# Kernel tuning notes

Measured on AMD Instinct MI355X. Metric: run time of the kernel, lower is better.

Reference implementation:

```python
import jax, jax.numpy as jnp
import numpy as np
from jax import lax

N_HEADS = 8
D_K = 64
D_V = 64
TEMP = float(np.sqrt(D_K))  # MixtureOfSoftMax temperature = d_k ** 0.5


def avg_pool_3x3_s2_same(x):
    """TF-style AveragePooling2D(pool=3, stride=2, padding='same'), NHWC.
    TF excludes padded elements from the average (divide by valid count)."""
    sums = lax.reduce_window(x, 0.0, lax.add, (1, 3, 3, 1), (1, 2, 2, 1), 'SAME')
    ones = jnp.ones(x.shape[:3] + (1,), x.dtype)
    cnt = lax.reduce_window(ones, 0.0, lax.add, (1, 3, 3, 1), (1, 2, 2, 1), 'SAME')
    return sums / cnt


def conv1x1(x, w, b):
    # 1x1 conv == per-pixel channel matmul
    return jnp.einsum('bhwc,cd->bhwd', x, w) + b


def setup_inputs() -> dict:
    key = jax.random.key(0)
    ks = jax.random.split(key, 6)
    C = 512
    s1 = float(np.sqrt(2.0 / (C + D_K)))  # init_weight1 std
    s3 = float(np.sqrt(2.0 / (C + D_V)))  # init_weight3 std
    return {
        'x':   jax.random.normal(ks[0], (4, 64, 64, C), jnp.float32),
        'w_q': jax.random.normal(ks[1], (C, N_HEADS * D_K), jnp.float32) * s1,
        'b_q': jnp.zeros((N_HEADS * D_K,), jnp.float32),
        'w_k': jax.random.normal(ks[2], (C, N_HEADS * D_K), jnp.float32) * s1,
        'b_k': jnp.zeros((N_HEADS * D_K,), jnp.float32),
        'w_v': jax.random.normal(ks[3], (C, N_HEADS * D_V), jnp.float32) * s3,
        'b_v': jnp.zeros((N_HEADS * D_V,), jnp.float32),
        'w_o': jax.random.normal(ks[4], (N_HEADS * D_V, C), jnp.float32) * 0.02,
        'b_o': jnp.zeros((C,), jnp.float32),
    }


def reference(x, w_q, b_q, w_k, b_k, w_v, b_v, w_o, b_o):
    BS, H, W, C = x.shape
    residual = x
    # Q from full-res x; K, V from 3x3/s2 average-pooled x (pooling=True)
    qt = conv1x1(x, w_q, b_q).reshape(BS * N_HEADS, H * W, -1)          # (B*h, N, d_k)
    xp = avg_pool_3x3_s2_same(x)                                         # (BS, H/2, W/2, C)
    kt = conv1x1(xp, w_k, b_k).reshape(BS * N_HEADS, H * W // 4, -1)     # (B*h, N/4, d_k)
    vt = conv1x1(xp, w_v, b_v).reshape(BS * N_HEADS, H * W // 4, -1)     # (B*h, N/4, d_v)
    # MixtureOfSoftMaxACF with n_mix=1: scaled dot-product softmax attention
    attn = jnp.einsum('bnd,bmd->bnm', qt, kt) / TEMP                     # (B*h, N, N/4)
    attn = jax.nn.softmax(attn, axis=-1)                                 # dropout=identity (inference)
    out = jnp.einsum('bnm,bmd->bnd', attn, vt)                           # (B*h, N, d_v)
    out = out.reshape(BS, H, W, -1)
    out = conv1x1(out, w_o, b_o)                                         # conv1x1_bn_relu (Conv2D only in call)
    return out + residual                                                # concat=False -> Add
```

## Files before the change

### kernel.cpp

```cpp
#include <hip/hip_runtime.h>
#include <hip/hip_bf16.h>
#include <math.h>

typedef short bf16x8 __attribute__((ext_vector_type(8)));
typedef float f32x4 __attribute__((ext_vector_type(4)));
typedef unsigned short u16;

__device__ inline float b2f(u16 h) {
    unsigned int u = ((unsigned int)h) << 16;
    float f;
    __builtin_memcpy(&f, &u, 4);
    return f;
}

__device__ inline u16 f2b(float f) {
    unsigned int u;
    __builtin_memcpy(&u, &f, 4);
    unsigned int lsb = (u >> 16) & 1u;
    u += 0x7fffu + lsb;
    return (u16)(u >> 16);
}

__device__ __forceinline__ void gl2lds16(const u16* g, u16* l) {
    __builtin_amdgcn_global_load_lds(
        (const __attribute__((address_space(1))) unsigned int*)g,
        (__attribute__((address_space(3))) unsigned int*)l,
        16, 0, 0);
}

#define PITCH 72

#define QSCALE 0.18033688011112042f

__global__ __launch_bounds__(256) void prep_kernel(const float* __restrict__ x,
                                                   const float* __restrict__ w0,
                                                   const float* __restrict__ w1,
                                                   const float* __restrict__ w2,
                                                   const float* __restrict__ w3,
                                                   u16* __restrict__ wt,
                                                   u16* __restrict__ xp) {
    __shared__ u16 T[64 * PITCH];
    int tid = threadIdx.x;
    if (blockIdx.x >= 256) {
        int idx = (blockIdx.x - 256) * 256 + tid;
        int c8 = idx & 63;
        int j = (idx >> 6) & 31;
        int i = (idx >> 11) & 31;
        int b = idx >> 16;
        int r0 = 2 * i, c0 = 2 * j;
        int rmax = min(r0 + 3, 64), cmax = min(c0 + 3, 64);
        float acc[8] = {};
        for (int r = r0; r < rmax; ++r)
            for (int cc = c0; cc < cmax; ++cc) {
                const float* p = &x[(size_t)((((b << 6) + r) << 6) + cc) * 512 + c8 * 8];
                float4 v0 = *(const float4*)p;
                float4 v1 = *(const float4*)(p + 4);
                acc[0] += v0.x; acc[1] += v0.y; acc[2] += v0.z; acc[3] += v0.w;
                acc[4] += v1.x; acc[5] += v1.y; acc[6] += v1.z; acc[7] += v1.w;
            }
        float inv = 1.f / (float)((rmax - r0) * (cmax - c0));
        u16 o[8];
#pragma unroll
        for (int t = 0; t < 8; ++t) o[t] = f2b(acc[t] * inv);
        *(int4*)(&xp[(size_t)idx * 8]) = *(int4*)o;
        return;
    }
    int t5 = blockIdx.x;
    int bx = t5 & 7, by = (t5 >> 3) & 7, bz = t5 >> 6;
    const float* W = bz == 0 ? w0 : bz == 1 ? w1 : bz == 2 ? w2 : w3;
    u16* WT = wt + (size_t)bz * 262144;
    int nB = bx * 64, kB = by * 64;
#pragma unroll
    for (int t = 0; t < 4; ++t) {
        int e = tid + t * 256;
        int r = e >> 4, c4 = (e & 15) * 4;
        float4 v = *(const float4*)(&W[(size_t)(kB + r) * 512 + nB + c4]);
        u16* dst = &T[r * PITCH + c4];
        dst[0] = f2b(v.x); dst[1] = f2b(v.y); dst[2] = f2b(v.z); dst[3] = f2b(v.w);
    }
    __syncthreads();
    int n = tid & 63, kg = tid >> 6;
#pragma unroll
    for (int p = 0; p < 2; ++p) {
        int k0 = (kg + p * 4) * 8;
        u16 tmp[8];
#pragma unroll
        for (int i = 0; i < 8; ++i) tmp[i] = T[(k0 + i) * PITCH + n];
        *(int4*)(&WT[(size_t)(nB + n) * 512 + kB + k0]) = *(int4*)tmp;
    }
}

template <int OM, int BN, int GY, bool AF32>
__device__ __forceinline__ void gemm_body(int bid,
                                          const void* __restrict__ Av,
                                          const u16* __restrict__ WT,
                                          const float* __restrict__ bias,
                                          const float* __restrict__ bias2res,
                                          void* __restrict__ Cv,
                                          void* __restrict__ Cv2,
                                          float oscale,
                                          u16* At, u16* Bt) {
    int tid = threadIdx.x, lane = tid & 63, wave = tid >> 6;
    int q = lane >> 4, l16 = lane & 15;
    constexpr int MI = (BN == 128) ? 2 : 1;
    int wm, wn;
    if constexpr (BN == 128) { wm = wave & 1; wn = wave >> 1; }
    else                     { wm = wave;     wn = 0; }
    int nBlk = bid / GY;
    int mBlk = bid - nBlk * GY;
    int nBase = nBlk * BN, mBase = mBlk * 64;
    f32x4 acc[MI][4] = {};

    for (int kk = 0; kk < 512; kk += 64) {
        __syncthreads();
        if constexpr (AF32) {
            const float* Af = (const float*)Av;
#pragma unroll
            for (int t = 0; t < 4; ++t) {
                int c = tid + t * 256;
                int m = c >> 4, kc = (c & 15) ^ (m & 15);
                gl2lds16((const u16*)&Af[(size_t)(mBase + m) * 512 + kk + kc * 4],
                         &At[c * 8]);
            }
        } else {
            const u16* Ab = (const u16*)Av;
#pragma unroll
            for (int t = 0; t < 2; ++t) {
                int c = tid + t * 256;
                int m = c >> 3, kc = (c & 7) ^ (m & 7);
                gl2lds16(&Ab[(size_t)(mBase + m) * 512 + kk + kc * 8], &At[c * 8]);
            }
        }
#pragma unroll
        for (int t = 0; t < BN / 32; ++t) {
            int c = tid + t * 256;
            int m = c >> 3, kc = (c & 7) ^ (m & 7);
            gl2lds16(&WT[(size_t)(nBase + m) * 512 + kk + kc * 8], &Bt[c * 8]);
        }
        __syncthreads();
#pragma unroll
        for (int ds = 0; ds < 2; ++ds) {
            bf16x8 a[MI], b[4];
#pragma unroll
            for (int i = 0; i < MI; ++i) {
                int ma = (BN == 128 ? wm * 32 : wm * 16) + i * 16 + l16;
                if constexpr (AF32) {
                    const float* Ar = (const float*)At + ma * 64;
                    int c0 = ((ds << 3) + (q << 1)) ^ (ma & 15);
                    int c1 = c0 ^ 1;
                    float4 v0 = *(const float4*)(Ar + c0 * 4);
                    float4 v1 = *(const float4*)(Ar + c1 * 4);
                    unsigned r0, r1, r2, r3;
                    asm("v_cvt_pk_bf16_f32 %0, %1, %2" : "=v"(r0) : "v"(v0.x), "v"(v0.y));
                    asm("v_cvt_pk_bf16_f32 %0, %1, %2" : "=v"(r1) : "v"(v0.z), "v"(v0.w));
                    asm("v_cvt_pk_bf16_f32 %0, %1, %2" : "=v"(r2) : "v"(v1.x), "v"(v1.y));
                    asm("v_cvt_pk_bf16_f32 %0, %1, %2" : "=v"(r3) : "v"(v1.z), "v"(v1.w));
                    int4 tmp;
                    tmp.x = (int)r0; tmp.y = (int)r1; tmp.z = (int)r2; tmp.w = (int)r3;
                    __builtin_memcpy(&a[i], &tmp, 16);
                } else {
                    a[i] = *(bf16x8*)(&At[ma * 64 + ((((ds << 2) + q) ^ (ma & 7)) << 3)]);
                }
            }
#pragma unroll
            for (int j = 0; j < 4; ++j) {
                int nb = wn * 64 + j * 16 + l16;
                b[j] = *(bf16x8*)(&Bt[nb * 64 + ((((ds << 2) + q) ^ (nb & 7)) << 3)]);
            }
#pragma unroll
            for (int i = 0; i < MI; ++i)
#pragma unroll
                for (int j = 0; j < 4; ++j)
                    acc[i][j] = __builtin_amdgcn_mfma_f32_16x16x32_bf16(a[i], b[j], acc[i][j], 0, 0, 0);
        }
    }

    bool isK = (OM != 3) || (nBase < 512);
#pragma unroll
    for (int j = 0; j < 4; ++j) {
        int col = nBase + wn * 64 + j * 16 + l16;
        float bv;
        if constexpr (OM == 3) bv = isK ? bias[col] : bias2res[col - 512];
        else bv = bias[col];
#pragma unroll
        for (int i = 0; i < MI; ++i) {
#pragma unroll
            for (int r = 0; r < 4; ++r) {
                int row = mBase + (BN == 128 ? wm * 32 : wm * 16) + i * 16 + q * 4 + r;
                float v = acc[i][j][r] + bv;
                if constexpr (OM == 1) {
                    v += bias2res[(size_t)row * 512 + col];
                    ((float*)Cv)[(size_t)row * 512 + col] = v;
                } else if constexpr (OM == 0) {
                    ((u16*)Cv)[(size_t)row * 512 + col] = f2b(v * oscale);
                } else {
                    if (isK) {
                        ((u16*)Cv)[(size_t)row * 512 + col] = f2b(v);
                    } else {
                        int colv = col - 512;
                        int g = row >> 7, m2 = ((row & 127) << 3) + (colv >> 6), d = colv & 63;
                        ((u16*)Cv2)[(size_t)((g << 6) + d) * 1024 + m2] = f2b(v);
                    }
                }
            }
        }
    }
}

__global__ __launch_bounds__(256, 4) void qkv_kernel(const float* __restrict__ x,
                                                     const u16* __restrict__ xp,
                                                     const u16* __restrict__ wT,
                                                     const float* __restrict__ b_q,
                                                     const float* __restrict__ b_k,
                                                     const float* __restrict__ b_v,
                                                     u16* __restrict__ Qw,
                                                     u16* __restrict__ Kw,
                                                     u16* __restrict__ VwT) {
    __shared__ __align__(16) u16 At[64 * 128];
    __shared__ __align__(16) u16 Bt[128 * 64];
    int gid = blockIdx.x;
    if (gid < 1024) {
        gemm_body<0, 128, 256, true>(gid, x, wT, b_q, nullptr, Qw, nullptr, QSCALE, At, Bt);
    } else {
        gemm_body<3, 64, 64, false>(gid - 1024, xp, wT + 262144, b_k, b_v, Kw, VwT, 1.0f, At, Bt);
    }
}

__global__ __launch_bounds__(256, 4) void gemm_o_kernel(const u16* __restrict__ Ow,
                                                        const u16* __restrict__ wTo,
                                                        const float* __restrict__ b_o,
                                                        const float* __restrict__ xres,
                                                        float* __restrict__ out) {
    __shared__ __align__(16) u16 At[64 * 64];
    __shared__ __align__(16) u16 Bt[128 * 64];
    gemm_body<1, 128, 256, false>(blockIdx.x, Ow, wTo, b_o, xres, out, nullptr, 1.0f, At, Bt);
}

__global__ __launch_bounds__(256, 4) void attn_kernel(const u16* __restrict__ Q,
                                                      const u16* __restrict__ K,
                                                      const u16* __restrict__ VT_g,
                                                      u16* __restrict__ O) {
    int g = blockIdx.x;
    int qtile = blockIdx.y;
    const u16* Qg = Q + (size_t)g * 262144;
    const u16* Kg = K + (size_t)g * 65536;
    const u16* Vt = VT_g + (size_t)g * 65536;
    u16* Og = O + (size_t)g * 262144;

    __shared__ __align__(16) u16 Kt[2][64 * 64];
    __shared__ __align__(16) u16 VTs[2][64 * 64];
    __shared__ __align__(16) u16 Pt[64 * 64];

    int tid = threadIdx.x, lane = tid & 63, wave = tid >> 6;
    int q = lane >> 4, l16 = lane & 15;
    int n0 = qtile * 128;
    int pkey = (l16 & 7) << 2;
    int prow = (wave * 16 + l16) * 32;
    int* Pt32 = (int*)Pt;

    bf16x8 qf[2][2];
#pragma unroll
    for (int s = 0; s < 2; ++s)
#pragma unroll
        for (int ds = 0; ds < 2; ++ds)
            qf[s][ds] = *(const bf16x8*)(
                &Qg[(size_t)(n0 + s * 64 + wave * 16 + l16) * 64 + ds * 32 + q * 8]);

    f32x4 oacc[2][4] = {};
    float rsum[2] = {0.f, 0.f};

    auto stage = [&](int buf, int kb) {
#pragma unroll
        for (int t = 0; t < 2; ++t) {
            int c = tid + t * 256;
            int m = c >> 3, kc = (c & 7) ^ (m & 7);
            gl2lds16(&Kg[(size_t)(kb * 64 + m) * 64 + kc * 8], &Kt[buf][c * 8]);
            gl2lds16(&Vt[(size_t)m * 1024 + kb * 64 + kc * 8], &VTs[buf][c * 8]);
        }
    };

    stage(0, 0);
    asm volatile("s_waitcnt vmcnt(0)" ::: "memory");
    __syncthreads();

    int cur = 0;
#pragma unroll 1
    for (int kb = 0; kb < 16; ++kb) {
        if (kb < 15) stage(cur ^ 1, kb + 1);
        const u16* KtB = Kt[cur];
        const u16* VTsB = VTs[cur];
#pragma unroll
        for (int s = 0; s < 2; ++s) {
#pragma unroll
            for (int cb = 0; cb < 4; ++cb) {
                int m = cb * 16 + l16;
                bf16x8 kf0 = *(const bf16x8*)(&KtB[m * 64 + ((q ^ (m & 7)) << 3)]);
                bf16x8 kf1 = *(const bf16x8*)(&KtB[m * 64 + (((4 + q) ^ (m & 7)) << 3)]);
                f32x4 z = {};
                __builtin_amdgcn_s_setprio(1);
                z = __builtin_amdgcn_mfma_f32_16x16x32_bf16(kf0, qf[s][0], z, 0, 0, 0);
                z = __builtin_amdgcn_mfma_f32_16x16x32_bf16(kf1, qf[s][1], z, 0, 0, 0);
                __builtin_amdgcn_s_setprio(0);
                float p0 = __builtin_amdgcn_exp2f(z[0]);
                float p1 = __builtin_amdgcn_exp2f(z[1]);
                float p2 = __builtin_amdgcn_exp2f(z[2]);
                float p3 = __builtin_amdgcn_exp2f(z[3]);
                rsum[s] += (p0 + p1) + (p2 + p3);
                unsigned w0, w1;
                asm("v_cvt_pk_bf16_f32 %0, %1, %2" : "=v"(w0) : "v"(p0), "v"(p1));
                asm("v_cvt_pk_bf16_f32 %0, %1, %2" : "=v"(w1) : "v"(p2), "v"(p3));
                int2 w;
                w.x = (int)w0;
                w.y = (int)w1;
                int pd = (cb * 8 + q * 2) ^ pkey;
                *(int2*)(&Pt32[prow + pd]) = w;
            }
#pragma unroll
            for (int ds = 0; ds < 2; ++ds) {
                int pd = (ds * 16 + q * 4) ^ pkey;
                bf16x8 ap = *(bf16x8*)(&Pt32[prow + pd]);
                __builtin_amdgcn_s_setprio(1);
#pragma unroll
                for (int db = 0; db < 4; ++db) {
                    int dd = db * 16 + l16;
                    int jj = ds * 4 + q;
                    bf16x8 vb = *(const bf16x8*)(&VTsB[dd * 64 + ((jj ^ (dd & 7)) << 3)]);
                    oacc[s][db] = __builtin_amdgcn_mfma_f32_16x16x32_bf16(ap, vb, oacc[s][db], 0, 0, 0);
                }
                __builtin_amdgcn_s_setprio(0);
            }
        }
        asm volatile("s_waitcnt vmcnt(0)" ::: "memory");
        __syncthreads();
        cur ^= 1;
    }

#pragma unroll
    for (int s = 0; s < 2; ++s) {
        float v = rsum[s];
        v += __shfl_xor(v, 16, 64);
        v += __shfl_xor(v, 32, 64);
        rsum[s] = v;
    }
    float inv[2][4];
#pragma unroll
    for (int s = 0; s < 2; ++s)
#pragma unroll
        for (int r = 0; r < 4; ++r)
            inv[s][r] = 1.f / __shfl(rsum[s], q * 4 + r, 64);
#pragma unroll
    for (int s = 0; s < 2; ++s)
#pragma unroll
        for (int db = 0; db < 4; ++db)
#pragma unroll
            for (int r = 0; r < 4; ++r) {
                int row = n0 + s * 64 + wave * 16 + q * 4 + r;
                Og[(size_t)row * 64 + db * 16 + l16] = f2b(oacc[s][db][r] * inv[s][r]);
            }
}

extern "C" void kernel_launch(void* const* d_in, const int* in_sizes, int n_in,
                              void* d_out, int out_size, void* d_ws, size_t ws_size,
                              hipStream_t stream) {
    const float* x   = (const float*)d_in[0];
    const float* w_q = (const float*)d_in[1];
    const float* b_q = (const float*)d_in[2];
    const float* w_k = (const float*)d_in[3];
    const float* b_k = (const float*)d_in[4];
    const float* w_v = (const float*)d_in[5];
    const float* b_v = (const float*)d_in[6];
    const float* w_o = (const float*)d_in[7];
    const float* b_o = (const float*)d_in[8];
    float* out = (float*)d_out;

    char* ws = (char*)d_ws;
    u16* Ow  = (u16*)(ws);
    u16* xp  = (u16*)(ws + (16ull << 20));
    u16* Qw  = (u16*)(ws + (20ull << 20));
    u16* Kw  = (u16*)(ws + (36ull << 20));
    u16* VwT = (u16*)(ws + (40ull << 20));
    u16* wT  = (u16*)(ws + (44ull << 20));

    prep_kernel<<<1280, 256, 0, stream>>>(x, w_q, w_k, w_v, w_o, wT, xp);
    qkv_kernel<<<2048, 256, 0, stream>>>(x, xp, wT, b_q, b_k, b_v, Qw, Kw, VwT);
    attn_kernel<<<dim3(32, 32), 256, 0, stream>>>(Qw, Kw, VwT, Ow);
    gemm_o_kernel<<<1024, 256, 0, stream>>>(Ow, wT + 786432, b_o, x, out);
}
```

Measured before the change: 194.5 us.

## Switch attention to 32x32x16 MFMA and keep P in registers via permlane32 swap

The attention kernel now uses 32x32x16 bf16 MFMA tiles, with each wave owning 32 query rows, in place of 16x16x32 tiles over two 64-row slices. The softmax probabilities are converted to bf16 and rearranged across lane halves with v_permlane32_swap so they can feed the P·V MFMA directly from registers. This removes the LDS round trip for P and the Pt shared buffer. The aim is to cut LDS traffic and instruction overhead, at the cost of more accumulator registers per wave and a more intricate lane mapping for rows and the row-sum reduction.

```diff
diff --git a/kernel.cpp b/kernel.cpp
--- a/kernel.cpp
+++ b/kernel.cpp
@@ -4,6 +4,7 @@
 
 typedef short bf16x8 __attribute__((ext_vector_type(8)));
 typedef float f32x4 __attribute__((ext_vector_type(4)));
+typedef float f32x16 __attribute__((ext_vector_type(16)));
 typedef unsigned short u16;
 
 __device__ inline float b2f(u16 h) {
@@ -249,25 +250,18 @@
 
     __shared__ __align__(16) u16 Kt[2][64 * 64];
     __shared__ __align__(16) u16 VTs[2][64 * 64];
-    __shared__ __align__(16) u16 Pt[64 * 64];
 
     int tid = threadIdx.x, lane = tid & 63, wave = tid >> 6;
-    int q = lane >> 4, l16 = lane & 15;
-    int n0 = qtile * 128;
-    int pkey = (l16 & 7) << 2;
-    int prow = (wave * 16 + l16) * 32;
-    int* Pt32 = (int*)Pt;
-
-    bf16x8 qf[2][2];
-#pragma unroll
-    for (int s = 0; s < 2; ++s)
-#pragma unroll
-        for (int ds = 0; ds < 2; ++ds)
-            qf[s][ds] = *(const bf16x8*)(
-                &Qg[(size_t)(n0 + s * 64 + wave * 16 + l16) * 64 + ds * 32 + q * 8]);
-
-    f32x4 oacc[2][4] = {};
-    float rsum[2] = {0.f, 0.f};
+    int l32 = lane & 31, h = lane >> 5;
+    int w0 = qtile * 128 + wave * 32;
+
+    bf16x8 qf[4];
+#pragma unroll
+    for (int j = 0; j < 4; ++j)
+        qf[j] = *(const bf16x8*)(&Qg[(size_t)(w0 + l32) * 64 + j * 16 + h * 8]);
+
+    f32x16 oacc[2] = {};
+    float rsum = 0.f;
 
     auto stage = [&](int buf, int kb) {
 #pragma unroll
@@ -290,73 +284,65 @@
         const u16* KtB = Kt[cur];
         const u16* VTsB = VTs[cur];
 #pragma unroll
-        for (int s = 0; s < 2; ++s) {
-#pragma unroll
-            for (int cb = 0; cb < 4; ++cb) {
-                int m = cb * 16 + l16;
-                bf16x8 kf0 = *(const bf16x8*)(&KtB[m * 64 + ((q ^ (m & 7)) << 3)]);
-                bf16x8 kf1 = *(const bf16x8*)(&KtB[m * 64 + (((4 + q) ^ (m & 7)) << 3)]);
-                f32x4 z = {};
-                __builtin_amdgcn_s_setprio(1);
-                z = __builtin_amdgcn_mfma_f32_16x16x32_bf16(kf0, qf[s][0], z, 0, 0, 0);
-                z = __builtin_amdgcn_mfma_f32_16x16x32_bf16(kf1, qf[s][1], z, 0, 0, 0);
-                __builtin_amdgcn_s_setprio(0);
-                float p0 = __builtin_amdgcn_exp2f(z[0]);
-                float p1 = __builtin_amdgcn_exp2f(z[1]);
-                float p2 = __builtin_amdgcn_exp2f(z[2]);
-                float p3 = __builtin_amdgcn_exp2f(z[3]);
-                rsum[s] += (p0 + p1) + (p2 + p3);
-                unsigned w0, w1;
-                asm("v_cvt_pk_bf16_f32 %0, %1, %2" : "=v"(w0) : "v"(p0), "v"(p1));
-                asm("v_cvt_pk_bf16_f32 %0, %1, %2" : "=v"(w1) : "v"(p2), "v"(p3));
-                int2 w;
-                w.x = (int)w0;
-                w.y = (int)w1;
-                int pd = (cb * 8 + q * 2) ^ pkey;
-                *(int2*)(&Pt32[prow + pd]) = w;
-            }
-#pragma unroll
-            for (int ds = 0; ds < 2; ++ds) {
-                int pd = (ds * 16 + q * 4) ^ pkey;
-                bf16x8 ap = *(bf16x8*)(&Pt32[prow + pd]);
-                __builtin_amdgcn_s_setprio(1);
-#pragma unroll
-                for (int db = 0; db < 4; ++db) {
-                    int dd = db * 16 + l16;
-                    int jj = ds * 4 + q;
-                    bf16x8 vb = *(const bf16x8*)(&VTsB[dd * 64 + ((jj ^ (dd & 7)) << 3)]);
-                    oacc[s][db] = __builtin_amdgcn_mfma_f32_16x16x32_bf16(ap, vb, oacc[s][db], 0, 0, 0);
+        for (int mb = 0; mb < 2; ++mb) {
+            int m = mb * 32 + l32;
+            f32x16 z = {};
+            __builtin_amdgcn_s_setprio(1);
+#pragma unroll
+            for (int j = 0; j < 4; ++j) {
+                int slot = (j * 2 + h) ^ (m & 7);
+                bf16x8 kf = *(const bf16x8*)(&KtB[m * 64 + slot * 8]);
+                z = __builtin_amdgcn_mfma_f32_32x32x16_bf16(kf, qf[j], z, 0, 0, 0);
+            }
+            __builtin_amdgcn_s_setprio(0);
+            float p[16];
+#pragma unroll
+            for (int e = 0; e < 16; ++e) {
+                p[e] = __builtin_amdgcn_exp2f(z[e]);
+                rsum += p[e];
+            }
+            unsigned D[8];
+#pragma unroll
+            for (int i = 0; i < 8; ++i)
+                asm("v_cvt_pk_bf16_f32 %0, %1, %2" : "=v"(D[i]) : "v"(p[2 * i]), "v"(p[2 * i + 1]));
+            asm("v_permlane32_swap_b32 %0, %1" : "+v"(D[2]), "+v"(D[0]));
+            asm("v_permlane32_swap_b32 %0, %1" : "+v"(D[3]), "+v"(D[1]));
+            asm("v_permlane32_swap_b32 %0, %1" : "+v"(D[6]), "+v"(D[4]));
+            asm("v_permlane32_swap_b32 %0, %1" : "+v"(D[7]), "+v"(D[5]));
+            bf16x8 fr[2];
+            __builtin_memcpy(&fr[0], &D[0], 16);
+            __builtin_memcpy(&fr[1], &D[4], 16);
+            __builtin_amdgcn_s_setprio(1);
+#pragma unroll
+            for (int ms = 0; ms < 2; ++ms)
+#pragma unroll
+                for (int db = 0; db < 2; ++db) {
+                    int d = db * 32 + l32;
+                    int c = mb * 4 + ms * 2 + h;
+                    bf16x8 vb = *(const bf16x8*)(&VTsB[d * 64 + ((c ^ (d & 7)) << 3)]);
+                    oacc[db] = __builtin_amdgcn_mfma_f32_32x32x16_bf16(fr[ms], vb, oacc[db], 0, 0, 0);
                 }
-                __builtin_amdgcn_s_setprio(0);
-            }
+            __builtin_amdgcn_s_setprio(0);
         }
         asm volatile("s_waitcnt vmcnt(0)" ::: "memory");
         __syncthreads();
         cur ^= 1;
     }
 
-#pragma unroll
-    for (int s = 0; s < 2; ++s) {
-        float v = rsum[s];
-        v += __shfl_xor(v, 16, 64);
-        v += __shfl_xor(v, 32, 64);
-        rsum[s] = v;
-    }
-    float inv[2][4];
-#pragma unroll
-    for (int s = 0; s < 2; ++s)
-#pragma unroll
-        for (int r = 0; r < 4; ++r)
-            inv[s][r] = 1.f / __shfl(rsum[s], q * 4 + r, 64);
-#pragma unroll
-    for (int s = 0; s < 2; ++s)
-#pragma unroll
-        for (int db = 0; db < 4; ++db)
-#pragma unroll
-            for (int r = 0; r < 4; ++r) {
-                int row = n0 + s * 64 + wave * 16 + q * 4 + r;
-                Og[(size_t)row * 64 + db * 16 + l16] = f2b(oacc[s][db][r] * inv[s][r]);
-            }
+    float rs = rsum + __shfl_xor(rsum, 32, 64);
+    float inv[16];
+#pragma unroll
+    for (int r = 0; r < 16; ++r) {
+        int row = (r & 3) + 8 * (r >> 2) + 4 * h;
+        inv[r] = 1.f / __shfl(rs, row, 64);
+    }
+#pragma unroll
+    for (int db = 0; db < 2; ++db)
+#pragma unroll
+        for (int r = 0; r < 16; ++r) {
+            int row = (r & 3) + 8 * (r >> 2) + 4 * h;
+            Og[(size_t)(w0 + row) * 64 + db * 32 + l32] = f2b(oacc[db][r] * inv[r]);
+        }
 }
 
 extern "C" void kernel_launch(void* const* d_in, const int* in_sizes, int n_in,
```

After: 188.4 us. 1.03x faster.
